# Kernel tuning notes

Hardware: AMD Instinct MI355X
Metric: run time of the kernel (lower is better)

The kernel has to match this reference:

```python
import jax, jax.numpy as jnp
import numpy as np

N = 100000   # num_nodes
R = 200      # num_relations
DIM = 200    # hidden dim (in = out for every layer)
B = 30       # num_bases
L = 2        # num_layers
E = 800000   # num_edges


def setup_inputs() -> dict:
    key = jax.random.key(0)
    ks = jax.random.split(key, 7)
    edge_index = jax.random.randint(ks[0], (2, E), 0, N)
    edge_type = jax.random.randint(ks[1], (E,), 0, R)
    s = 1.0 / np.sqrt(DIM)
    emb = jax.random.normal(ks[2], (N, DIM), jnp.float32)
    comp = jax.random.normal(ks[3], (L, R, B), jnp.float32) * (1.0 / np.sqrt(B))
    bases = jax.random.normal(ks[4], (L, B, DIM, DIM), jnp.float32) * s
    root = jax.random.normal(ks[5], (L, DIM, DIM), jnp.float32) * s
    bias = jnp.zeros((L, DIM), jnp.float32)
    return dict(edge_index=edge_index, edge_type=edge_type, emb=emb,
                comp=comp, bases=bases, root=root, bias=bias)


def _rgcn_layer(x, src, dst, etype, comp_l, bases_l, root_l, bias_l):
    # Basis decomposition: W_r = sum_b comp[r, b] * bases[b]
    # msg_e = x[src_e] @ W_{etype_e}  computed as sum over bases (B is small & fixed)
    x_src = x[src]                      # [E, DIM] gather
    c = comp_l[etype]                   # [E, B] per-edge basis coefficients

    def body(acc, bc):
        basis_b, c_b = bc               # [DIM, DIM], [E]
        return acc + c_b[:, None] * (x_src @ basis_b), None

    acc0 = jnp.zeros((x_src.shape[0], root_l.shape[1]), x.dtype)
    msg, _ = jax.lax.scan(body, acc0, (bases_l, jnp.swapaxes(c, 0, 1)))  # [E, DIM]

    # PyG RGCNConv mean aggregation: normalize by in-degree per (dst node, relation)
    comb = dst * R + etype
    deg = jax.ops.segment_sum(jnp.ones((etype.shape[0],), x.dtype), comb,
                              num_segments=N * R)
    norm = 1.0 / jnp.maximum(deg[comb], 1.0)                             # [E]

    agg = jax.ops.segment_sum(msg * norm[:, None], dst, num_segments=N)  # [N, DIM]
    return agg + x @ root_l + bias_l


def reference(edge_index, edge_type, emb, comp, bases, root, bias):
    src, dst = edge_index[0], edge_index[1]
    x = emb
    for l in range(L):
        x = jax.nn.relu(_rgcn_layer(x, src, dst, edge_type,
                                    comp[l], bases[l], root[l], bias[l]))
        # dropout is identity in eval mode (deterministic reference)
    return x
```

## Files before the change

### kernel.cpp

```cpp
#include <hip/hip_runtime.h>
#include <hip/hip_bf16.h>
#include <stdint.h>

#define NN 100000
#define RR 200
#define DD 200
#define BB 30
#define LL 2
#define EE 800000

#define KP 224
#define NP 208
#define XP 224
#define AP 232
#define BPP 232
#define RT 128
#define MSGP 200
#define NSPL 2
#define MAXNC 24
#define NPART 128
#define EPB ((EE + NPART - 1) / NPART)

using bf16x8 = __attribute__((ext_vector_type(8))) short;
using f32x4  = __attribute__((ext_vector_type(4))) float;

#define OFF_NORM   0ull
#define OFF_SORT   3200000ull
#define OFF_CNT    6400000ull
#define OFF_XB     6404096ull
#define OFF_WT     51204096ull
#define OFF_ROOTT  69840896ull
#define OFF_CTL    69934080ull
#define OFF_POS    70065152ull
#define OFF_DSTCNT 73265152ull
#define OFF_DSTST  73665152ull
#define OFF_CUR    74065184ull
#define OFF_BLKH   74465184ull

static __device__ __forceinline__ short f2bf(float v) {
    union { __hip_bfloat16 h; short s; } u;
    u.h = __float2bfloat16(v);
    return u.s;
}

__global__ void kCount(const int* __restrict__ ei, const int* __restrict__ et,
                       unsigned int* __restrict__ deg8, int* __restrict__ dstCnt, int big) {
    int e = blockIdx.x * 256 + threadIdx.x;
    if (e >= EE) return;
    int d = ei[EE + e];
    int t = et[e];
    int comb = d * RR + t;
    atomicAdd(&deg8[comb >> 2], 1u << ((comb & 3) * 8));
    if (big) atomicAdd(&dstCnt[d], 1);
}

__global__ void kScanBlk(const int* __restrict__ dstCnt, int* __restrict__ dstStart,
                         int* __restrict__ blkSum) {
    __shared__ int s[256];
    int t = threadIdx.x, i = blockIdx.x * 256 + t;
    int v = (i < NN) ? dstCnt[i] : 0;
    s[t] = v;
    __syncthreads();
    #pragma unroll
    for (int off = 1; off < 256; off <<= 1) {
        int x = (t >= off) ? s[t - off] : 0;
        __syncthreads();
        s[t] += x;
        __syncthreads();
    }
    if (i < NN) dstStart[i] = s[t] - v;
    if (t == 255) blkSum[blockIdx.x] = s[255];
}
__global__ void kScanTop(int* __restrict__ blkSum, int nblk) {
    __shared__ int s[512];
    int t = threadIdx.x;
    int v = (t < nblk) ? blkSum[t] : 0;
    s[t] = v;
    __syncthreads();
    #pragma unroll
    for (int off = 1; off < 512; off <<= 1) {
        int x = (t >= off) ? s[t - off] : 0;
        __syncthreads();
        s[t] += x;
        __syncthreads();
    }
    if (t < nblk) blkSum[t] = s[t] - v;
}
__global__ void kScanAdd(const int* __restrict__ dstCnt, int* __restrict__ dstStart,
                         const int* __restrict__ blkSum) {
    int i = blockIdx.x * 256 + threadIdx.x;
    if (i >= NN) return;
    int v = dstStart[i] + blkSum[blockIdx.x];
    dstStart[i] = v;
    if (i == NN - 1) dstStart[NN] = v + dstCnt[i];
}

__global__ void kChunk(const int* __restrict__ dstStart, int* __restrict__ bS,
                       int* __restrict__ cesS, int NC, int T) {
    int tid = threadIdx.x;
    if (tid > NC) return;
    int v;
    if (tid == NC) v = NN;
    else if (tid == 0) v = 0;
    else {
        int target = tid * T;
        int lo = 0, hi = NN;
        while (lo < hi) {
            int mid = (lo + hi) >> 1;
            if (dstStart[mid] >= target) hi = mid; else lo = mid + 1;
        }
        v = lo;
    }
    bS[tid] = v;
    cesS[tid] = dstStart[v];
}

__global__ __launch_bounds__(256) void kHist(const int* __restrict__ ei,
        const int* __restrict__ et, const int* __restrict__ bS,
        int* __restrict__ blockHist, int NC) {
    __shared__ int hist[MAXNC * RR];
    __shared__ int bsh[MAXNC + 1];
    int tid = threadIdx.x, b = blockIdx.x;
    int NB = NC * RR;
    if (tid <= NC) bsh[tid] = bS[tid];
    for (int i = tid; i < NB; i += 256) hist[i] = 0;
    __syncthreads();
    int ebeg = b * EPB, eend = min(EE, ebeg + EPB);
    for (int e = ebeg + tid; e < eend; e += 256) {
        int d = ei[EE + e];
        int t = et[e];
        int c = 0;
        for (int j = 1; j < NC; ++j) if (d >= bsh[j]) c = j;
        atomicAdd(&hist[c * RR + t], 1);
    }
    __syncthreads();
    for (int i = tid; i < NB; i += 256)
        blockHist[(size_t)b * NB + i] = hist[i];
}

__global__ __launch_bounds__(128) void kScanP(int* __restrict__ blockHist,
                                              int* __restrict__ cntB, int NB) {
    __shared__ int s[NPART];
    int t = threadIdx.x, k = blockIdx.x;
    int v = blockHist[(size_t)t * NB + k];
    s[t] = v;
    __syncthreads();
    #pragma unroll
    for (int off = 1; off < NPART; off <<= 1) {
        int x = (t >= off) ? s[t - off] : 0;
        __syncthreads();
        s[t] += x;
        __syncthreads();
    }
    blockHist[(size_t)t * NB + k] = s[t] - v;
    if (t == NPART - 1) cntB[k] = s[NPART - 1];
}

__global__ void kScanB(const int* __restrict__ cntB, int* __restrict__ relStartB,
                       int* __restrict__ cursorB, int nb) {
    __shared__ int c[MAXNC * RR];
    __shared__ int rs[MAXNC * RR + 1];
    int tid = threadIdx.x;
    for (int i = tid; i < nb; i += 256) c[i] = cntB[i];
    __syncthreads();
    if (tid == 0) {
        int s = 0;
        for (int i = 0; i < nb; ++i) {
            rs[i] = s;
            s += c[i];
        }
        rs[nb] = s;
    }
    __syncthreads();
    for (int i = tid; i <= nb; i += 256) {
        relStartB[i] = rs[i];
        if (i < nb) cursorB[i] = rs[i];
    }
}

__global__ __launch_bounds__(256) void kPart(const int* __restrict__ ei,
        const int* __restrict__ et, const unsigned int* __restrict__ deg8,
        const int* __restrict__ bS, const int* __restrict__ relStartB,
        const int* __restrict__ blockHist, const int* __restrict__ dstStart,
        int* __restrict__ cur, float* __restrict__ norm, int* __restrict__ sortedE,
        int* __restrict__ posDst, int NC) {
    __shared__ int curL[MAXNC * RR];
    __shared__ int bsh[MAXNC + 1];
    int tid = threadIdx.x, b = blockIdx.x;
    int NB = NC * RR;
    if (tid <= NC) bsh[tid] = bS[tid];
    for (int i = tid; i < NB; i += 256)
        curL[i] = relStartB[i] + blockHist[(size_t)b * NB + i];
    __syncthreads();
    int ebeg = b * EPB, eend = min(EE, ebeg + EPB);
    for (int e = ebeg + tid; e < eend; e += 256) {
        int d = ei[EE + e];
        int t = et[e];
        int comb = d * RR + t;
        unsigned int deg = (deg8[comb >> 2] >> ((comb & 3) * 8)) & 0xffu;
        norm[e] = 1.0f / (float)(deg ? deg : 1u);
        int c = 0;
        for (int j = 1; j < NC; ++j) if (d >= bsh[j]) c = j;
        int pos = atomicAdd(&curL[c * RR + t], 1);
        sortedE[pos] = e;
        posDst[e] = dstStart[d] + atomicAdd(&cur[d], 1);
    }
}

__global__ void kCountB(const int* __restrict__ ei, const int* __restrict__ et,
                        const int* __restrict__ bS, int* __restrict__ cntB, int NC) {
    __shared__ int bsh[MAXNC + 1];
    if (threadIdx.x <= NC) bsh[threadIdx.x] = bS[threadIdx.x];
    __syncthreads();
    int e = blockIdx.x * 256 + threadIdx.x;
    if (e >= EE) return;
    int d = ei[EE + e];
    int t = et[e];
    int c = 0;
    for (int j = 1; j < NC; ++j) if (d >= bsh[j]) c = j;
    atomicAdd(&cntB[c * RR + t], 1);
}

__global__ void kNormScatter(const int* __restrict__ ei, const int* __restrict__ et,
                             const unsigned int* __restrict__ deg8, const int* __restrict__ bS,
                             int* __restrict__ cursorB, const int* __restrict__ dstStart,
                             int* __restrict__ cur, float* __restrict__ norm,
                             int* __restrict__ sortedE, int* __restrict__ posDst,
                             int NC, int big) {
    __shared__ int bsh[MAXNC + 1];
    if (threadIdx.x <= NC) bsh[threadIdx.x] = bS[threadIdx.x];
    __syncthreads();
    int e = blockIdx.x * 256 + threadIdx.x;
    if (e >= EE) return;
    int d = ei[EE + e];
    int t = et[e];
    int comb = d * RR + t;
    unsigned int deg = (deg8[comb >> 2] >> ((comb & 3) * 8)) & 0xffu;
    norm[e] = 1.0f / (float)(deg ? deg : 1u);
    int c = 0;
    for (int j = 1; j < NC; ++j) if (d >= bsh[j]) c = j;
    int pos = atomicAdd(&cursorB[c * RR + t], 1);
    sortedE[pos] = e;
    if (big) posDst[e] = dstStart[d] + atomicAdd(&cur[d], 1);
}

__global__ void kConvert(const float* __restrict__ x, short* __restrict__ xb, int doRelu) {
    int idx = blockIdx.x * 256 + threadIdx.x;
    if (idx >= NN * XP) return;
    int i = idx / XP, col = idx - i * XP;
    float v = 0.0f;
    if (col < DD) {
        v = x[i * DD + col];
        if (doRelu) v = fmaxf(v, 0.0f);
    }
    xb[idx] = (col < DD) ? f2bf(v) : (short)0;
}

__global__ void kRelu(float* __restrict__ y) {
    int idx = blockIdx.x * 256 + threadIdx.x;
    if (idx < NN * DD) y[idx] = fmaxf(y[idx], 0.0f);
}

__global__ __launch_bounds__(256) void kW(const float* __restrict__ comp,
                                          const float* __restrict__ bases,
                                          short* __restrict__ Wt) {
    int kt = blockIdx.x;
    int ng = blockIdx.y;
    int tid = threadIdx.x;
    int k = kt * 32 + (tid & 31);
    int n = ng * 8 + (tid >> 5);
    bool live = (k < DD) && (n < DD);
    float vb[BB];
    #pragma unroll
    for (int b = 0; b < BB; ++b)
        vb[b] = live ? bases[((size_t)b * DD + k) * DD + n] : 0.0f;
    size_t wo = (size_t)n * KP + k;
    for (int r = 0; r < RR; ++r) {
        float a = 0.0f;
        #pragma unroll
        for (int b = 0; b < BB; ++b) a += comp[r * BB + b] * vb[b];
        Wt[(size_t)r * (NP * KP) + wo] = f2bf(a);
    }
}

__global__ void kRootT(const float* __restrict__ root, short* __restrict__ rootT) {
    int idx = blockIdx.x * 256 + threadIdx.x;
    if (idx >= NP * KP) return;
    int n = idx / KP, k = idx - n * KP;
    rootT[idx] = (n < DD && k < DD) ? f2bf(root[k * DD + n]) : (short)0;
}

template<int F0, int NF>
__device__ __forceinline__ void gemmHalf2(const short* As, const short* bCol,
                                          int arow0, int arow1, int kg,
                                          f32x4* acc0, f32x4* acc1) {
    #pragma unroll
    for (int f = 0; f < NF; ++f) {
        acc0[f] = (f32x4){0.f, 0.f, 0.f, 0.f};
        acc1[f] = (f32x4){0.f, 0.f, 0.f, 0.f};
    }
    bf16x8 bb[2][NF];
    #pragma unroll
    for (int f = 0; f < NF; ++f)
        bb[0][f] = *(const bf16x8*)(bCol + (size_t)(F0 + f) * 16 * KP);
    #pragma unroll
    for (int kc = 0; kc < 7; ++kc) {
        if (kc < 6) {
            #pragma unroll
            for (int f = 0; f < NF; ++f)
                bb[(kc + 1) & 1][f] = *(const bf16x8*)(bCol + (size_t)(F0 + f) * 16 * KP + (kc + 1) * 32);
        }
        bf16x8 a0 = *(const bf16x8*)(&As[arow0 * AP + kc * 32 + kg]);
        bf16x8 a1 = *(const bf16x8*)(&As[arow1 * AP + kc * 32 + kg]);
        #pragma unroll
        for (int f = 0; f < NF; ++f) {
            acc0[f] = __builtin_amdgcn_mfma_f32_16x16x32_bf16(a0, bb[kc & 1][f], acc0[f], 0, 0, 0);
            acc1[f] = __builtin_amdgcn_mfma_f32_16x16x32_bf16(a1, bb[kc & 1][f], acc1[f], 0, 0, 0);
        }
    }
}

__global__ __launch_bounds__(256) void kRootGemm(const short* __restrict__ xb,
        const short* __restrict__ rootT, const float* __restrict__ bias,
        float* __restrict__ y) {
    __shared__ short As[RT * AP];
    int i0 = blockIdx.x * RT;
    int tid = threadIdx.x;
    int rowL = tid >> 1, sub = tid & 1;
    int i = i0 + rowL;
    for (int c = sub; c < 28; c += 2) {
        int4 v = make_int4(0, 0, 0, 0);
        if (i < NN) v = *(const int4*)(xb + (size_t)i * XP + c * 8);
        *(int4*)(&As[rowL * AP + c * 8]) = v;
    }
    __syncthreads();
    int lane = tid & 63, wave = tid >> 6;
    int arow0 = wave * 32 + (lane & 15);
    int arow1 = arow0 + 16;
    int kg = (lane >> 4) * 8;
    const short* bCol = rootT + (lane & 15) * KP + kg;
    int colLane = lane & 15;
    int rbase = i0 + wave * 32 + (lane >> 4) * 4;
    {
        f32x4 acc0[7], acc1[7];
        gemmHalf2<0, 7>(As, bCol, arow0, arow1, kg, acc0, acc1);
        #pragma unroll
        for (int f = 0; f < 7; ++f) {
            int col = f * 16 + colLane;
            float bv = bias[col];
            #pragma unroll
            for (int j = 0; j < 4; ++j) {
                int r0 = rbase + j, r1 = rbase + 16 + j;
                if (r0 < NN) y[(size_t)r0 * DD + col] = acc0[f][j] + bv;
                if (r1 < NN) y[(size_t)r1 * DD + col] = acc1[f][j] + bv;
            }
        }
    }
    {
        f32x4 acc0[6], acc1[6];
        gemmHalf2<7, 6>(As, bCol, arow0, arow1, kg, acc0, acc1);
        #pragma unroll
        for (int f = 0; f < 6; ++f) {
            int col = (7 + f) * 16 + colLane;
            if (col < DD) {
                float bv = bias[col];
                #pragma unroll
                for (int j = 0; j < 4; ++j) {
                    int r0 = rbase + j, r1 = rbase + 16 + j;
                    if (r0 < NN) y[(size_t)r0 * DD + col] = acc0[f][j] + bv;
                    if (r1 < NN) y[(size_t)r1 * DD + col] = acc1[f][j] + bv;
                }
            }
        }
    }
}

template<int MODE>
__global__ __launch_bounds__(512) void kMsgP(const int* __restrict__ ei,
        const short* __restrict__ xb, const short* __restrict__ Wt,
        const int* __restrict__ relStartB, const int* __restrict__ sortedE,
        const float* __restrict__ norm, const int* __restrict__ posDst,
        const int* __restrict__ cesS, float* __restrict__ y,
        short* __restrict__ msg, int c) {
    __shared__ short Bp[NP * BPP];
    int r = blockIdx.x / NSPL;
    int h = blockIdx.x - r * NSPL;
    int relStart = relStartB[c * RR + r];
    int eEnd     = relStartB[c * RR + r + 1];
    int nE = eEnd - relStart;
    if (nE <= 0) return;
    int tid = threadIdx.x;
    {
        const short* wp = Wt + (size_t)r * (NP * KP);
        for (int idx = tid; idx < NP * (KP / 8); idx += 512) {
            int n = idx / (KP / 8);
            int k8 = idx - n * (KP / 8);
            int4 v = *(const int4*)(wp + (size_t)n * KP + k8 * 8);
            *(int4*)(&Bp[n * BPP + k8 * 8]) = v;
        }
    }
    __syncthreads();
    int lane = tid & 63, wave = tid >> 6;
    int colLane = lane & 15;
    int kg = (lane >> 4) * 8;
    int rbase = (lane >> 4) * 4;
    int nwt = (nE + 31) / 32;
    int ces = (MODE == 0) ? cesS[c] : 0;

    bf16x8 aC[2][7], aN[2][7];
    int psC[2][4], psN[2][4];
    float nmC[2][4], nmN[2][4];

    auto loadTile = [&](int wt, bf16x8 (*a)[7], int (*ps)[4], float (*nm)[4]) {
        int eBase = relStart + wt * 32;
        #pragma unroll
        for (int m = 0; m < 2; ++m) {
            int eIdxA = eBase + m * 16 + colLane;
            int eidA = sortedE[min(eIdxA, eEnd - 1)];
            int srcA = ei[eidA];
            const short* aRow = xb + (size_t)srcA * XP;
            #pragma unroll
            for (int kc = 0; kc < 7; ++kc)
                a[m][kc] = *(const bf16x8*)(aRow + kc * 32 + kg);
            #pragma unroll
            for (int j = 0; j < 4; ++j) {
                int eI = eBase + m * 16 + rbase + j;
                bool v = eI < eEnd;
                int eid = v ? sortedE[eI] : 0;
                nm[m][j] = v ? norm[eid] : 0.0f;
                if (MODE == 0) ps[m][j] = v ? (posDst[eid] - ces) : -1;
                else           ps[m][j] = v ? ei[EE + eid] : -1;
            }
        }
    };

    int wt = h * 8 + wave;
    if (wt < nwt) loadTile(wt, aC, psC, nmC);
    for (; wt < nwt; wt += NSPL * 8) {
        int wtn = wt + NSPL * 8;
        if (wtn < nwt) loadTile(wtn, aN, psN, nmN);
        {
            f32x4 acc0[7], acc1[7];
            #pragma unroll
            for (int f = 0; f < 7; ++f) {
                acc0[f] = (f32x4){0.f, 0.f, 0.f, 0.f};
                acc1[f] = (f32x4){0.f, 0.f, 0.f, 0.f};
            }
            #pragma unroll
            for (int kc = 0; kc < 7; ++kc) {
                bf16x8 bb[7];
                #pragma unroll
                for (int f = 0; f < 7; ++f)
                    bb[f] = *(const bf16x8*)(&Bp[(f * 16 + colLane) * BPP + kc * 32 + kg]);
                #pragma unroll
                for (int f = 0; f < 7; ++f) {
                    acc0[f] = __builtin_amdgcn_mfma_f32_16x16x32_bf16(aC[0][kc], bb[f], acc0[f], 0, 0, 0);
                    acc1[f] = __builtin_amdgcn_mfma_f32_16x16x32_bf16(aC[1][kc], bb[f], acc1[f], 0, 0, 0);
                }
            }
            #pragma unroll
            for (int m = 0; m < 2; ++m) {
                #pragma unroll
                for (int j = 0; j < 4; ++j) {
                    int ps = psC[m][j]; float nm = nmC[m][j];
                    if (ps >= 0) {
                        #pragma unroll
                        for (int f = 0; f < 7; ++f) {
                            int col = f * 16 + colLane;
                            float val = (m ? acc1[f][j] : acc0[f][j]) * nm;
                            if (MODE == 0) msg[(size_t)ps * MSGP + col] = f2bf(val);
                            else           atomicAdd(&y[(size_t)ps * DD + col], val);
                        }
                    }
                }
            }
        }
        {
            f32x4 acc0[6], acc1[6];
            #pragma unroll
            for (int f = 0; f < 6; ++f) {
                acc0[f] = (f32x4){0.f, 0.f, 0.f, 0.f};
                acc1[f] = (f32x4){0.f, 0.f, 0.f, 0.f};
            }
            #pragma unroll
            for (int kc = 0; kc < 7; ++kc) {
                bf16x8 bb[6];
                #pragma unroll
                for (int f = 0; f < 6; ++f)
                    bb[f] = *(const bf16x8*)(&Bp[((7 + f) * 16 + colLane) * BPP + kc * 32 + kg]);
                #pragma unroll
                for (int f = 0; f < 6; ++f) {
                    acc0[f] = __builtin_amdgcn_mfma_f32_16x16x32_bf16(aC[0][kc], bb[f], acc0[f], 0, 0, 0);
                    acc1[f] = __builtin_amdgcn_mfma_f32_16x16x32_bf16(aC[1][kc], bb[f], acc1[f], 0, 0, 0);
                }
            }
            #pragma unroll
            for (int m = 0; m < 2; ++m) {
                #pragma unroll
                for (int j = 0; j < 4; ++j) {
                    int ps = psC[m][j]; float nm = nmC[m][j];
                    if (ps >= 0) {
                        #pragma unroll
                        for (int f = 0; f < 6; ++f) {
                            int col = (7 + f) * 16 + colLane;
                            if (col < DD) {
                                float val = (m ? acc1[f][j] : acc0[f][j]) * nm;
                                if (MODE == 0) msg[(size_t)ps * MSGP + col] = f2bf(val);
                                else           atomicAdd(&y[(size_t)ps * DD + col], val);
                            }
                        }
                    }
                }
            }
        }
        if (wtn < nwt) {
            #pragma unroll
            for (int m = 0; m < 2; ++m) {
                #pragma unroll
                for (int kc = 0; kc < 7; ++kc) aC[m][kc] = aN[m][kc];
                #pragma unroll
                for (int j = 0; j < 4; ++j) { psC[m][j] = psN[m][j]; nmC[m][j] = nmN[m][j]; }
            }
        }
    }
}

__global__ __launch_bounds__(256) void kAgg(const short* __restrict__ msg,
        const int* __restrict__ dstStart, const int* __restrict__ bS,
        const int* __restrict__ cesS, float* __restrict__ y, int c) {
    int wv = threadIdx.x >> 6, lane = threadIdx.x & 63;
    int b0 = bS[c], b1 = bS[c + 1];
    int ces = cesS[c];
    int gw = blockIdx.x * 4 + wv;
    int nw = gridDim.x * 4;
    for (int d = b0 + gw; d < b1; d += nw) {
        int s = dstStart[d] - ces, e = dstStart[d + 1] - ces;
        float a0 = 0.f, a1 = 0.f, a2 = 0.f, a3 = 0.f;
        if (lane < 50) {
            for (int j = s; j < e; ++j) {
                int2 v = *(const int2*)(msg + (size_t)j * MSGP + lane * 4);
                unsigned u0 = (unsigned)v.x, u1 = (unsigned)v.y;
                a0 += __uint_as_float(u0 << 16);
                a1 += __uint_as_float(u0 & 0xffff0000u);
                a2 += __uint_as_float(u1 << 16);
                a3 += __uint_as_float(u1 & 0xffff0000u);
            }
            int colBase = lane * 4;
            float4 rv = *(const float4*)(y + (size_t)d * DD + colBase);
            float4 o;
            o.x = fmaxf(rv.x + a0, 0.f);
            o.y = fmaxf(rv.y + a1, 0.f);
            o.z = fmaxf(rv.z + a2, 0.f);
            o.w = fmaxf(rv.w + a3, 0.f);
            *(float4*)(y + (size_t)d * DD + colBase) = o;
        }
    }
}

extern "C" void kernel_launch(void* const* d_in, const int* in_sizes, int n_in,
                              void* d_out, int out_size, void* d_ws, size_t ws_size,
                              hipStream_t stream) {
    (void)in_sizes; (void)n_in; (void)out_size;
    const int*   ei    = (const int*)d_in[0];
    const int*   et    = (const int*)d_in[1];
    const float* emb   = (const float*)d_in[2];
    const float* comp  = (const float*)d_in[3];
    const float* bases = (const float*)d_in[4];
    const float* root  = (const float*)d_in[5];
    const float* bias  = (const float*)d_in[6];
    float* y = (float*)d_out;
    char* ws = (char*)d_ws;
    float* norm    = (float*)(ws + OFF_NORM);
    int*   sortedE = (int*)(ws + OFF_SORT);
    short* xb      = (short*)(ws + OFF_XB);
    short* Wt      = (short*)(ws + OFF_WT);
    short* rootT   = (short*)(ws + OFF_ROOTT);
    int*   posDst  = (int*)(ws + OFF_POS);
    int*   dstCnt  = (int*)(ws + OFF_DSTCNT);
    int*   dstStart= (int*)(ws + OFF_DSTST);
    int*   cur     = (int*)(ws + OFF_CUR);
    int*   blockHist = (int*)(ws + OFF_BLKH);
    unsigned int* deg8 = (unsigned int*)(ws + OFF_XB);

    int NC = 0;
    long long T = EE;
    unsigned long long msgOff = 0;
    for (int cc = 1; cc <= MAXNC; ++cc) {
        long long t = (EE + cc - 1) / cc;
        unsigned long long mo = OFF_BLKH + (unsigned long long)NPART * cc * RR * 4;
        unsigned long long need = mo + (unsigned long long)(t + 64) * (MSGP * 2);
        if ((unsigned long long)ws_size >= need) { NC = cc; T = t; msgOff = mo; break; }
    }
    int big = (NC > 0) ? 1 : 0;
    if (!big) { NC = 1; T = EE; msgOff = OFF_BLKH; }
    short* msg = (short*)(ws + msgOff);

    int *cntB, *relStartB, *cursorB, *bS, *cesS, *blkSum;
    if (big) {
        int* ctl = (int*)(ws + OFF_CTL);
        cntB = ctl; relStartB = ctl + 4864; cursorB = ctl + 9728;
        bS = ctl + 19456; cesS = ctl + 19520; blkSum = ctl + 19584;
    } else {
        int* ctl = (int*)(ws + OFF_CNT);
        cntB = ctl; relStartB = ctl + 256; cursorB = ctl + 512;
        bS = ctl + 976; cesS = ctl + 992; blkSum = ctl + 1000;
    }

    const int NBLK = (NN + 255) / 256;

    hipMemsetAsync(deg8, 0, (size_t)NN * RR, stream);
    if (big) {
        hipMemsetAsync(dstCnt, 0, (size_t)NN * 4, stream);
        hipMemsetAsync(cur, 0, (size_t)NN * 4, stream);
    } else {
        hipMemsetAsync((void*)cntB, 0, 4096, stream);
    }

    kCount<<<(EE + 255) / 256, 256, 0, stream>>>(ei, et, deg8, dstCnt, big);
    if (big) {
        kScanBlk<<<NBLK, 256, 0, stream>>>(dstCnt, dstStart, blkSum);
        kScanTop<<<1, 512, 0, stream>>>(blkSum, NBLK);
        kScanAdd<<<NBLK, 256, 0, stream>>>(dstCnt, dstStart, blkSum);
        kChunk<<<1, 64, 0, stream>>>(dstStart, bS, cesS, NC, (int)T);
        kHist<<<NPART, 256, 0, stream>>>(ei, et, bS, blockHist, NC);
        kScanP<<<NC * RR, NPART, 0, stream>>>(blockHist, cntB, NC * RR);
        kScanB<<<1, 256, 0, stream>>>(cntB, relStartB, cursorB, NC * RR);
        kPart<<<NPART, 256, 0, stream>>>(ei, et, deg8, bS, relStartB, blockHist,
                                         dstStart, cur, norm, sortedE, posDst, NC);
    } else {
        kCountB<<<(EE + 255) / 256, 256, 0, stream>>>(ei, et, bS, cntB, NC);
        kScanB<<<1, 256, 0, stream>>>(cntB, relStartB, cursorB, NC * RR);
        kNormScatter<<<(EE + 255) / 256, 256, 0, stream>>>(ei, et, deg8, bS, cursorB,
                                                           dstStart, cur, norm, sortedE,
                                                           posDst, NC, big);
    }
    kConvert<<<(NN * XP + 255) / 256, 256, 0, stream>>>(emb, xb, 0);

    for (int l = 0; l < LL; ++l) {
        kW<<<dim3(7, 26), 256, 0, stream>>>(comp + l * RR * BB,
                                            bases + (size_t)l * BB * DD * DD, Wt);
        kRootT<<<(NP * KP + 255) / 256, 256, 0, stream>>>(root + l * DD * DD, rootT);
        kRootGemm<<<(NN + RT - 1) / RT, 256, 0, stream>>>(xb, rootT, bias + l * DD, y);
        if (big) {
            for (int c = 0; c < NC; ++c) {
                kMsgP<0><<<RR * NSPL, 512, 0, stream>>>(ei, xb, Wt, relStartB, sortedE,
                                                        norm, posDst, cesS, y, msg, c);
                kAgg<<<2048, 256, 0, stream>>>(msg, dstStart, bS, cesS, y, c);
            }
            if (l == 0)
                kConvert<<<(NN * XP + 255) / 256, 256, 0, stream>>>(y, xb, 0);
        } else {
            kMsgP<1><<<RR * NSPL, 512, 0, stream>>>(ei, xb, Wt, relStartB, sortedE,
                                                    norm, posDst, cesS, y, msg, 0);
            if (l == 0) kConvert<<<(NN * XP + 255) / 256, 256, 0, stream>>>(y, xb, 1);
            else        kRelu<<<(NN * DD + 255) / 256, 256, 0, stream>>>(y);
        }
    }
}
```

Before: 1.263 ms.

## Split msg GEMM across blocks by output columns instead of edge tiles

The two blocks per relation now each own half of the output columns (7 or 6 column tiles) and process all edge tiles, instead of splitting edge tiles between them. Each block stages only its half of the relation weight in shared memory, which halves LDS use and adds a launch bound of 4 blocks per CU to raise occupancy. In exchange, every block gathers every source row, so the A-operand gathers and index/norm loads are duplicated across the two blocks.

```diff
diff --git a/kernel.cpp b/kernel.cpp
--- a/kernel.cpp
+++ b/kernel.cpp
@@ -375,24 +375,68 @@
     }
 }
 
+template<int MODE, int F0, int NF>
+__device__ __forceinline__ void msgCompute(const short* Bp,
+        const bf16x8 (&aC)[2][7], const int (&psC)[2][4], const float (&nmC)[2][4],
+        int colLane, int kg, short* __restrict__ msg, float* __restrict__ y) {
+    f32x4 acc0[NF], acc1[NF];
+    #pragma unroll
+    for (int f = 0; f < NF; ++f) {
+        acc0[f] = (f32x4){0.f, 0.f, 0.f, 0.f};
+        acc1[f] = (f32x4){0.f, 0.f, 0.f, 0.f};
+    }
+    #pragma unroll
+    for (int kc = 0; kc < 7; ++kc) {
+        bf16x8 bb[NF];
+        #pragma unroll
+        for (int f = 0; f < NF; ++f)
+            bb[f] = *(const bf16x8*)(&Bp[(f * 16 + colLane) * BPP + kc * 32 + kg]);
+        #pragma unroll
+        for (int f = 0; f < NF; ++f) {
+            acc0[f] = __builtin_amdgcn_mfma_f32_16x16x32_bf16(aC[0][kc], bb[f], acc0[f], 0, 0, 0);
+            acc1[f] = __builtin_amdgcn_mfma_f32_16x16x32_bf16(aC[1][kc], bb[f], acc1[f], 0, 0, 0);
+        }
+    }
+    #pragma unroll
+    for (int m = 0; m < 2; ++m) {
+        #pragma unroll
+        for (int j = 0; j < 4; ++j) {
+            int ps = psC[m][j]; float nm = nmC[m][j];
+            if (ps >= 0) {
+                #pragma unroll
+                for (int f = 0; f < NF; ++f) {
+                    int col = (F0 + f) * 16 + colLane;
+                    if (col < DD) {
+                        float val = (m ? acc1[f][j] : acc0[f][j]) * nm;
+                        if (MODE == 0) msg[(size_t)ps * MSGP + col] = f2bf(val);
+                        else           atomicAdd(&y[(size_t)ps * DD + col], val);
+                    }
+                }
+            }
+        }
+    }
+}
+
 template<int MODE>
-__global__ __launch_bounds__(512) void kMsgP(const int* __restrict__ ei,
+__global__ __launch_bounds__(512, 4) void kMsgP(const int* __restrict__ ei,
         const short* __restrict__ xb, const short* __restrict__ Wt,
         const int* __restrict__ relStartB, const int* __restrict__ sortedE,
         const float* __restrict__ norm, const int* __restrict__ posDst,
         const int* __restrict__ cesS, float* __restrict__ y,
         short* __restrict__ msg, int c) {
-    __shared__ short Bp[NP * BPP];
-    int r = blockIdx.x / NSPL;
-    int h = blockIdx.x - r * NSPL;
+    __shared__ short Bp[112 * BPP];
+    int r = blockIdx.x >> 1;
+    int h = blockIdx.x & 1;
     int relStart = relStartB[c * RR + r];
     int eEnd     = relStartB[c * RR + r + 1];
     int nE = eEnd - relStart;
     if (nE <= 0) return;
     int tid = threadIdx.x;
+    const int f0   = h ? 7 : 0;
+    const int nrow = h ? 96 : 112;
     {
-        const short* wp = Wt + (size_t)r * (NP * KP);
-        for (int idx = tid; idx < NP * (KP / 8); idx += 512) {
+        const short* wp = Wt + (size_t)r * (NP * KP) + (size_t)f0 * 16 * KP;
+        for (int idx = tid; idx < nrow * (KP / 8); idx += 512) {
             int n = idx / (KP / 8);
             int k8 = idx - n * (KP / 8);
             int4 v = *(const int4*)(wp + (size_t)n * KP + k8 * 8);
@@ -434,85 +478,13 @@
         }
     };
 
-    int wt = h * 8 + wave;
+    int wt = wave;
     if (wt < nwt) loadTile(wt, aC, psC, nmC);
-    for (; wt < nwt; wt += NSPL * 8) {
-        int wtn = wt + NSPL * 8;
+    for (; wt < nwt; wt += 8) {
+        int wtn = wt + 8;
         if (wtn < nwt) loadTile(wtn, aN, psN, nmN);
-        {
-            f32x4 acc0[7], acc1[7];
-            #pragma unroll
-            for (int f = 0; f < 7; ++f) {
-                acc0[f] = (f32x4){0.f, 0.f, 0.f, 0.f};
-                acc1[f] = (f32x4){0.f, 0.f, 0.f, 0.f};
-            }
-            #pragma unroll
-            for (int kc = 0; kc < 7; ++kc) {
-                bf16x8 bb[7];
-                #pragma unroll
-                for (int f = 0; f < 7; ++f)
-                    bb[f] = *(const bf16x8*)(&Bp[(f * 16 + colLane) * BPP + kc * 32 + kg]);
-                #pragma unroll
-                for (int f = 0; f < 7; ++f) {
-                    acc0[f] = __builtin_amdgcn_mfma_f32_16x16x32_bf16(aC[0][kc], bb[f], acc0[f], 0, 0, 0);
-                    acc1[f] = __builtin_amdgcn_mfma_f32_16x16x32_bf16(aC[1][kc], bb[f], acc1[f], 0, 0, 0);
-                }
-            }
-            #pragma unroll
-            for (int m = 0; m < 2; ++m) {
-                #pragma unroll
-                for (int j = 0; j < 4; ++j) {
-                    int ps = psC[m][j]; float nm = nmC[m][j];
-                    if (ps >= 0) {
-                        #pragma unroll
-                        for (int f = 0; f < 7; ++f) {
-                            int col = f * 16 + colLane;
-                            float val = (m ? acc1[f][j] : acc0[f][j]) * nm;
-                            if (MODE == 0) msg[(size_t)ps * MSGP + col] = f2bf(val);
-                            else           atomicAdd(&y[(size_t)ps * DD + col], val);
-                        }
-                    }
-                }
-            }
-        }
-        {
-            f32x4 acc0[6], acc1[6];
-            #pragma unroll
-            for (int f = 0; f < 6; ++f) {
-                acc0[f] = (f32x4){0.f, 0.f, 0.f, 0.f};
-                acc1[f] = (f32x4){0.f, 0.f, 0.f, 0.f};
-            }
-            #pragma unroll
-            for (int kc = 0; kc < 7; ++kc) {
-                bf16x8 bb[6];
-                #pragma unroll
-                for (int f = 0; f < 6; ++f)
-                    bb[f] = *(const bf16x8*)(&Bp[((7 + f) * 16 + colLane) * BPP + kc * 32 + kg]);
-                #pragma unroll
-                for (int f = 0; f < 6; ++f) {
-                    acc0[f] = __builtin_amdgcn_mfma_f32_16x16x32_bf16(aC[0][kc], bb[f], acc0[f], 0, 0, 0);
-                    acc1[f] = __builtin_amdgcn_mfma_f32_16x16x32_bf16(aC[1][kc], bb[f], acc1[f], 0, 0, 0);
-                }
-            }
-            #pragma unroll
-            for (int m = 0; m < 2; ++m) {
-                #pragma unroll
-                for (int j = 0; j < 4; ++j) {
-                    int ps = psC[m][j]; float nm = nmC[m][j];
-                    if (ps >= 0) {
-                        #pragma unroll
-                        for (int f = 0; f < 6; ++f) {
-                            int col = (7 + f) * 16 + colLane;
-                            if (col < DD) {
-                                float val = (m ? acc1[f][j] : acc0[f][j]) * nm;
-                                if (MODE == 0) msg[(size_t)ps * MSGP + col] = f2bf(val);
-                                else           atomicAdd(&y[(size_t)ps * DD + col], val);
-                            }
-                        }
-                    }
-                }
-            }
-        }
+        if (h == 0) msgCompute<MODE, 0, 7>(Bp, aC, psC, nmC, colLane, kg, msg, y);
+        else        msgCompute<MODE, 7, 6>(Bp, aC, psC, nmC, colLane, kg, msg, y);
         if (wtn < nwt) {
             #pragma unroll
             for (int m = 0; m < 2; ++m) {
```

Measured after the change: 2.032 ms. 60.9% more time.
